# Kernel optimization log

Measured on AMD Instinct MI355X. Metric: run time of the kernel, lower is better.

Reference implementation:

```python
import jax, jax.numpy as jnp
import numpy as np

N = 100000   # nodes
E = 1600000  # edges
G = 512      # graphs
IN_F = 128
HID = 64
EPS = 1e-5


def setup_inputs() -> dict:
    key = jax.random.key(0)
    ks = jax.random.split(key, 16)
    x = jax.random.normal(ks[0], (N, IN_F), dtype=jnp.float32)
    edge_index = jax.random.randint(ks[1], (2, E), 0, N, dtype=jnp.int64)
    batch = jnp.sort(jax.random.randint(ks[2], (N,), 0, G, dtype=jnp.int64))
    s = 0.05
    return {
        'x': x, 'edge_index': edge_index, 'batch': batch,
        'W1': jax.random.normal(ks[3], (IN_F, HID), jnp.float32) * s,
        'b1': jax.random.normal(ks[4], (HID,), jnp.float32) * s,
        'g1': jax.random.uniform(ks[5], (HID,), jnp.float32),
        'be1': jax.random.normal(ks[6], (HID,), jnp.float32) * s,
        'rm1': jnp.zeros((HID,), jnp.float32),
        'rv1': jnp.ones((HID,), jnp.float32),
        'W2': jax.random.normal(ks[7], (HID, HID), jnp.float32) * s,
        'b2': jax.random.normal(ks[8], (HID,), jnp.float32) * s,
        'g2': jax.random.uniform(ks[9], (HID,), jnp.float32),
        'be2': jax.random.normal(ks[10], (HID,), jnp.float32) * s,
        'rm2': jnp.zeros((HID,), jnp.float32),
        'rv2': jnp.ones((HID,), jnp.float32),
        'Wh1': jax.random.normal(ks[11], (2 * HID, HID), jnp.float32) * s,
        'bh1': jax.random.normal(ks[12], (HID,), jnp.float32) * s,
        'Wh2': jax.random.normal(ks[13], (HID, HID // 2), jnp.float32) * s,
        'bh2': jnp.zeros((HID // 2,), jnp.float32),
        'Wh3': jax.random.normal(ks[14], (HID // 2, 1), jnp.float32) * s,
        'bh3': jnp.zeros((1,), jnp.float32),
    }


def _gcn(h, W, b, src, dst):
    # GCNConv with added self-loops and symmetric D^{-1/2} A D^{-1/2} normalization
    hw = h @ W                                   # [N, HID]
    deg = jnp.ones((N,), hw.dtype).at[dst].add(1.0)  # in-degree + self-loop
    dinv = jax.lax.rsqrt(deg)
    norm = dinv[src] * dinv[dst]                 # [E]
    agg = jax.ops.segment_sum(hw[src] * norm[:, None], dst, num_segments=N)
    return agg + hw * (dinv * dinv)[:, None] + b  # self-loop term + bias


def _bn(x, g, b, rm, rv):
    return (x - rm) * jax.lax.rsqrt(rv + EPS) * g + b


def reference(x, edge_index, batch, W1, b1, g1, be1, rm1, rv1,
              W2, b2, g2, be2, rm2, rv2, Wh1, bh1, Wh2, bh2, Wh3, bh3):
    src, dst = edge_index[0], edge_index[1]
    # layer 0 (no residual: dim change 128 -> 64)
    h = jax.nn.relu(_bn(_gcn(x, W1, b1, src, dst), g1, be1, rm1, rv1))
    # layer 1 with residual
    h = h + jax.nn.relu(_bn(_gcn(h, W2, b2, src, dst), g2, be2, rm2, rv2))
    # global mean + max pooling per graph
    ones = jnp.ones((N,), h.dtype)
    cnt = jnp.maximum(jax.ops.segment_sum(ones, batch, num_segments=G), 1.0)
    h_mean = jax.ops.segment_sum(h, batch, num_segments=G) / cnt[:, None]
    h_max = jax.ops.segment_max(h, batch, num_segments=G)
    hg = jnp.concatenate([h_mean, h_max], axis=-1)   # [G, 2*HID]
    # MLP head (dropout disabled in eval)
    z = jax.nn.relu(hg @ Wh1 + bh1)
    z = jax.nn.relu(z @ Wh2 + bh2)
    out = z @ Wh3 + bh3
    return jax.nn.sigmoid(out).squeeze(-1)           # [G]
```

## Files before the change

kernel.cpp:

```cpp
#include <hip/hip_runtime.h>
#include <math.h>

#define NN 100000
#define EE 1600000
#define GG 512
#define INF_ 128
#define HID 64
#define EPS 1e-5f

#define NBUK 391
#define P1_TILES 98

typedef unsigned int uint32;
typedef __attribute__((ext_vector_type(8))) short bf16x8;
typedef __attribute__((ext_vector_type(4))) float f32x4;

static __device__ inline uint32 f2bf(float f) {
    uint32 u = __float_as_uint(f);
    return (u + 0x7FFFu + ((u >> 16) & 1u)) >> 16;
}
static __device__ inline float bf_lo(uint32 u) { return __uint_as_float(u << 16); }
static __device__ inline float bf_hi(uint32 u) { return __uint_as_float(u & 0xFFFF0000u); }


__global__ __launch_bounds__(256) void k_bhist(const int* __restrict__ ei,
                                               int* __restrict__ bcnt) {
    __shared__ int h[NBUK];
    int t = threadIdx.x;
    for (int i = t; i < NBUK; i += 256) h[i] = 0;
    __syncthreads();
    const int4* dst4 = (const int4*)(ei + EE);
    int base4 = blockIdx.x * 4096;
    for (int j = 0; j < 16; ++j) {
        int i4 = base4 + j * 256 + t;
        if (i4 < EE / 4) {
            int4 d = dst4[i4];
            atomicAdd(&h[d.x >> 8], 1);
            atomicAdd(&h[d.y >> 8], 1);
            atomicAdd(&h[d.z >> 8], 1);
            atomicAdd(&h[d.w >> 8], 1);
        }
    }
    __syncthreads();
    for (int i = t; i < NBUK; i += 256)
        if (h[i]) atomicAdd(&bcnt[i], h[i]);
}

__global__ void k_bscan(const int* __restrict__ bcnt, int* __restrict__ bbase,
                        int* __restrict__ gcur, int* __restrict__ offs) {
    __shared__ int wsum[8];
    int t = threadIdx.x;
    int lane = t & 63, w = t >> 6;
    int c = (t < NBUK) ? bcnt[t] : 0;
    int v = c;
    for (int d = 1; d < 64; d <<= 1) { int n = __shfl_up(v, d); if (lane >= d) v += n; }
    if (lane == 63) wsum[w] = v;
    __syncthreads();
    int pre = 0;
    for (int q = 0; q < w; ++q) pre += wsum[q];
    int excl = pre + v - c;
    if (t <= NBUK) {
        bbase[t] = excl;
        if (t < NBUK) gcur[t] = excl;
    }
    if (t == 0) offs[NN] = EE;
}

__global__ __launch_bounds__(256) void k_p1(const int* __restrict__ ei,
                                            int* __restrict__ gcur,
                                            uint32* __restrict__ pairs) {
    __shared__ int h[NBUK];
    int t = threadIdx.x;
    for (int i = t; i < NBUK; i += 256) h[i] = 0;
    __syncthreads();
    const int4* src4 = (const int4*)ei;
    const int4* dst4 = (const int4*)(ei + EE);
    int base4 = blockIdx.x * 4096;
    for (int j = 0; j < 16; ++j) {
        int i4 = base4 + j * 256 + t;
        if (i4 < EE / 4) {
            int4 d = dst4[i4];
            atomicAdd(&h[d.x >> 8], 1);
            atomicAdd(&h[d.y >> 8], 1);
            atomicAdd(&h[d.z >> 8], 1);
            atomicAdd(&h[d.w >> 8], 1);
        }
    }
    __syncthreads();
    for (int i = t; i < NBUK; i += 256) {
        int c = h[i];
        h[i] = c ? atomicAdd(&gcur[i], c) : 0;
    }
    __syncthreads();
    for (int j = 0; j < 16; ++j) {
        int i4 = base4 + j * 256 + t;
        if (i4 < EE / 4) {
            int4 d = dst4[i4];
            int4 s = src4[i4];
            int p0 = atomicAdd(&h[d.x >> 8], 1);
            pairs[p0] = ((uint32)s.x << 8) | (uint32)(d.x & 255);
            int p1 = atomicAdd(&h[d.y >> 8], 1);
            pairs[p1] = ((uint32)s.y << 8) | (uint32)(d.y & 255);
            int p2 = atomicAdd(&h[d.z >> 8], 1);
            pairs[p2] = ((uint32)s.z << 8) | (uint32)(d.z & 255);
            int p3 = atomicAdd(&h[d.w >> 8], 1);
            pairs[p3] = ((uint32)s.w << 8) | (uint32)(d.w & 255);
        }
    }
}

__global__ __launch_bounds__(256) void k_p2(const uint32* __restrict__ pairs,
                                            const int* __restrict__ bbase,
                                            int* __restrict__ offs, float* __restrict__ dinv,
                                            int* __restrict__ col) {
    int b = blockIdx.x, t = threadIdx.x;
    int nbase = b << 8;
    int ebase = bbase[b], eend = bbase[b + 1];
    int m = eend - ebase;
    __shared__ int cnt[256];
    __shared__ int wsum[4];
    cnt[t] = 0;
    __syncthreads();
    for (int i = t; i < m; i += 256)
        atomicAdd(&cnt[pairs[ebase + i] & 255u], 1);
    __syncthreads();
    int c = cnt[t];
    int lane = t & 63, w = t >> 6;
    int v = c;
    for (int d = 1; d < 64; d <<= 1) { int n = __shfl_up(v, d); if (lane >= d) v += n; }
    if (lane == 63) wsum[w] = v;
    __syncthreads();
    int pre = 0;
    for (int q = 0; q < w; ++q) pre += wsum[q];
    int excl = pre + v - c;
    int node = nbase + t;
    if (node < NN) {
        offs[node] = ebase + excl;
        dinv[node] = rsqrtf(1.f + (float)c);
    }
    __syncthreads();
    cnt[t] = excl;
    __syncthreads();
    for (int i = t; i < m; i += 256) {
        uint32 u = pairs[ebase + i];
        int loc = atomicAdd(&cnt[u & 255u], 1);
        col[ebase + loc] = (int)(u >> 8);
    }
}

__global__ void k_setup(const float* b1, const float* g1, const float* be1,
                        const float* rm1, const float* rv1,
                        const float* b2, const float* g2, const float* be2,
                        const float* rm2, const float* rv2, float* sc,
                        const float* W1, uint32* Wt1b,
                        const float* W2, uint32* Wt2b, int* bcnt) {
    int i = blockIdx.x * 256 + threadIdx.x;
    if (i < 4096) {
        int n = i >> 6, kp = (i & 63) * 2;
        Wt1b[i] = f2bf(W1[(size_t)kp * 64 + n]) | (f2bf(W1[(size_t)(kp + 1) * 64 + n]) << 16);
    } else if (i < 6144) {
        int j = i - 4096;
        int n = j >> 5, kp = (j & 31) * 2;
        Wt2b[j] = f2bf(W2[(size_t)kp * 64 + n]) | (f2bf(W2[(size_t)(kp + 1) * 64 + n]) << 16);
    } else if (i < 6208) {
        int l = i - 6144;
        float s1 = g1[l] * rsqrtf(rv1[l] + EPS);
        sc[l]       = s1;
        sc[64 + l]  = (b1[l] - rm1[l]) * s1 + be1[l];
        float s2 = g2[l] * rsqrtf(rv2[l] + EPS);
        sc[128 + l] = s2;
        sc[192 + l] = (b2[l] - rm2[l]) * s2 + be2[l];
    } else if (i < 6208 + NBUK) {
        bcnt[i - 6208] = 0;
    }
}

template <int K>
__global__ __launch_bounds__(256) void k_gemm_mfma(const float* __restrict__ X,
                                                   const uint32* __restrict__ Wtb,
                                                   uint32* __restrict__ outb, int nrows) {
    constexpr int KP = K + 8;
    __shared__ alignas(16) unsigned short Al[64 * KP];
    __shared__ alignas(16) unsigned short Bl[64 * KP];
    int tid = threadIdx.x;
    for (int i = tid; i < 64 * (K / 2); i += 256) {
        int n = i / (K / 2), kp = i % (K / 2);
        *(uint32*)&Bl[n * KP + kp * 2] = Wtb[i];
    }
    int r0 = blockIdx.x * 64;
    const float* Xb = X + (size_t)r0 * K;
    int limit = (nrows - r0) * K;
    for (int f = tid * 4; f < 64 * K; f += 1024) {
        float4 v = {0.f, 0.f, 0.f, 0.f};
        if (f + 3 < limit) v = *(const float4*)&Xb[f];
        int row = f / K, kpos = f % K;
        ushort4 pk;
        pk.x = (unsigned short)f2bf(v.x);
        pk.y = (unsigned short)f2bf(v.y);
        pk.z = (unsigned short)f2bf(v.z);
        pk.w = (unsigned short)f2bf(v.w);
        *(ushort4*)&Al[row * KP + kpos] = pk;
    }
    __syncthreads();
    int lane = tid & 63, wv = tid >> 6;
    int m = lane & 15, quad = lane >> 4;
    f32x4 acc0 = {0.f, 0.f, 0.f, 0.f}, acc1 = acc0, acc2 = acc0, acc3 = acc0;
    int arow = wv * 16 + m;
#pragma unroll
    for (int k0 = 0; k0 < K; k0 += 32) {
        int koff = k0 + quad * 8;
        bf16x8 a = *(const bf16x8*)&Al[arow * KP + koff];
        bf16x8 b0 = *(const bf16x8*)&Bl[(0 * 16 + m) * KP + koff];
        bf16x8 b1 = *(const bf16x8*)&Bl[(1 * 16 + m) * KP + koff];
        bf16x8 b2 = *(const bf16x8*)&Bl[(2 * 16 + m) * KP + koff];
        bf16x8 b3 = *(const bf16x8*)&Bl[(3 * 16 + m) * KP + koff];
        acc0 = __builtin_amdgcn_mfma_f32_16x16x32_bf16(a, b0, acc0, 0, 0, 0);
        acc1 = __builtin_amdgcn_mfma_f32_16x16x32_bf16(a, b1, acc1, 0, 0, 0);
        acc2 = __builtin_amdgcn_mfma_f32_16x16x32_bf16(a, b2, acc2, 0, 0, 0);
        acc3 = __builtin_amdgcn_mfma_f32_16x16x32_bf16(a, b3, acc3, 0, 0, 0);
    }
    const float* accs[4] = {(const float*)&acc0, (const float*)&acc1,
                            (const float*)&acc2, (const float*)&acc3};
#pragma unroll
    for (int nt = 0; nt < 4; ++nt) {
#pragma unroll
        for (int reg = 0; reg < 4; ++reg) {
            float val = accs[nt][reg];
            float nxt = __shfl_down(val, 1);
            int row = r0 + wv * 16 + quad * 4 + reg;
            if (((m & 1) == 0) && row < nrows)
                outb[(size_t)row * 32 + nt * 8 + (m >> 1)] =
                    f2bf(val) | (f2bf(nxt) << 16);
        }
    }
}

__global__ void k_gcn_gather(const uint32* __restrict__ hwb, const int* __restrict__ col,
                             const int* __restrict__ offs,
                             const float* __restrict__ dinv, const float* __restrict__ scale,
                             const float* __restrict__ shift, const float* __restrict__ resid,
                             float* __restrict__ out) {
    int node = blockIdx.x * 4 + (threadIdx.x >> 6);
    if (node >= NN) return;
    int lane = threadIdx.x & 63;
    int half = lane >> 5;
    int fl = lane & 31;
    int e0 = offs[node], e1 = offs[node + 1];
    float di = dinv[node];
    float ax0 = 0.f, ay0 = 0.f, ax1 = 0.f, ay1 = 0.f;
    for (int base = e0; base < e1; base += 64) {
        int m = e1 - base; if (m > 64) m = 64;
        int srcv = 0; float wv = 0.f;
        if (lane < m) { srcv = col[base + lane]; wv = dinv[srcv]; }
        for (int j = 0; j < m; j += 8) {
            int   s0 = __shfl(srcv, j + half);
            int   s1 = __shfl(srcv, j + 2 + half);
            int   s2 = __shfl(srcv, j + 4 + half);
            int   s3 = __shfl(srcv, j + 6 + half);
            float w0 = __shfl(wv, j + half);
            float w1 = __shfl(wv, j + 2 + half);
            float w2 = __shfl(wv, j + 4 + half);
            float w3 = __shfl(wv, j + 6 + half);
            uint32 u0 = hwb[(size_t)s0 * 32 + fl];
            uint32 u1 = hwb[(size_t)s1 * 32 + fl];
            uint32 u2 = hwb[(size_t)s2 * 32 + fl];
            uint32 u3 = hwb[(size_t)s3 * 32 + fl];
            ax0 = fmaf(bf_lo(u0), w0, ax0); ay0 = fmaf(bf_hi(u0), w0, ay0);
            ax1 = fmaf(bf_lo(u1), w1, ax1); ay1 = fmaf(bf_hi(u1), w1, ay1);
            ax0 = fmaf(bf_lo(u2), w2, ax0); ay0 = fmaf(bf_hi(u2), w2, ay0);
            ax1 = fmaf(bf_lo(u3), w3, ax1); ay1 = fmaf(bf_hi(u3), w3, ay1);
        }
    }
    float ax = ax0 + ax1, ay = ay0 + ay1;
    ax += __shfl(ax, fl + 32);
    ay += __shfl(ay, fl + 32);
    if (half == 0) {
        uint32 uself = hwb[(size_t)node * 32 + fl];
        float dii = di * di;
        float vx = fmaf(ax * di + bf_lo(uself) * dii, scale[2 * fl],     shift[2 * fl]);
        float vy = fmaf(ay * di + bf_hi(uself) * dii, scale[2 * fl + 1], shift[2 * fl + 1]);
        vx = fmaxf(vx, 0.f);
        vy = fmaxf(vy, 0.f);
        if (resid) {
            float2 rv = *(const float2*)&resid[(size_t)node * 64 + 2 * fl];
            vx += rv.x; vy += rv.y;
        }
        float2 o; o.x = vx; o.y = vy;
        *(float2*)&out[(size_t)node * 64 + 2 * fl] = o;
    }
}

__global__ void k_pool(const float* __restrict__ h, const int* __restrict__ batch,
                       float* __restrict__ msum, float* __restrict__ mmax,
                       float* __restrict__ gcnt) {
    int lane = threadIdx.x;
    int i0 = blockIdx.x * 128;
    int i1 = i0 + 128; if (i1 > NN) i1 = NN;
    int cur = batch[i0];
    float sum = 0.f, mx = 0.f; int c = 0;
    for (int i = i0; i < i1; ++i) {
        int g = batch[i];
        if (g != cur) {
            atomicAdd(&msum[cur * 64 + lane], sum);
            atomicMax((unsigned int*)&mmax[cur * 64 + lane], __float_as_uint(mx));
            if (lane == 0) atomicAdd(&gcnt[cur], (float)c);
            sum = 0.f; mx = 0.f; c = 0; cur = g;
        }
        float v = h[(long)i * 64 + lane];
        sum += v; mx = fmaxf(mx, v); ++c;
    }
    atomicAdd(&msum[cur * 64 + lane], sum);
    atomicMax((unsigned int*)&mmax[cur * 64 + lane], __float_as_uint(mx));
    if (lane == 0) atomicAdd(&gcnt[cur], (float)c);
}

__global__ void k_head(const float* __restrict__ msum, const float* __restrict__ mmax,
                       const float* __restrict__ gcnt,
                       const float* __restrict__ Wh1, const float* __restrict__ bh1,
                       const float* __restrict__ Wh2, const float* __restrict__ bh2,
                       const float* __restrict__ Wh3, const float* __restrict__ bh3,
                       float* __restrict__ out) {
    int g = blockIdx.x, t = threadIdx.x;
    __shared__ float hg[128];
    __shared__ float z1[64];
    __shared__ float z2[32];
    float c = fmaxf(gcnt[g], 1.f);
    hg[t]      = msum[g * 64 + t] / c;
    hg[64 + t] = mmax[g * 64 + t];
    __syncthreads();
    float acc = bh1[t];
#pragma unroll 8
    for (int k = 0; k < 128; ++k) acc = fmaf(hg[k], Wh1[k * 64 + t], acc);
    z1[t] = fmaxf(acc, 0.f);
    __syncthreads();
    if (t < 32) {
        float a2 = bh2[t];
#pragma unroll 8
        for (int k = 0; k < 64; ++k) a2 = fmaf(z1[k], Wh2[k * 32 + t], a2);
        z2[t] = fmaxf(a2, 0.f);
    }
    __syncthreads();
    if (t == 0) {
        float a3 = bh3[0];
        for (int k = 0; k < 32; ++k) a3 = fmaf(z2[k], Wh3[k], a3);
        out[g] = 1.f / (1.f + expf(-a3));
    }
}


static inline size_t alignup(size_t x) { return (x + 255) & ~(size_t)255; }

extern "C" void kernel_launch(void* const* d_in, const int* in_sizes, int n_in,
                              void* d_out, int out_size, void* d_ws, size_t ws_size,
                              hipStream_t stream) {
    const float* x   = (const float*)d_in[0];
    const int*   ei  = (const int*)d_in[1];
    const int*   bat = (const int*)d_in[2];
    const float* W1  = (const float*)d_in[3];
    const float* b1  = (const float*)d_in[4];
    const float* g1  = (const float*)d_in[5];
    const float* be1 = (const float*)d_in[6];
    const float* rm1 = (const float*)d_in[7];
    const float* rv1 = (const float*)d_in[8];
    const float* W2  = (const float*)d_in[9];
    const float* b2  = (const float*)d_in[10];
    const float* g2  = (const float*)d_in[11];
    const float* be2 = (const float*)d_in[12];
    const float* rm2 = (const float*)d_in[13];
    const float* rv2 = (const float*)d_in[14];
    const float* Wh1 = (const float*)d_in[15];
    const float* bh1 = (const float*)d_in[16];
    const float* Wh2 = (const float*)d_in[17];
    const float* bh2 = (const float*)d_in[18];
    const float* Wh3 = (const float*)d_in[19];
    const float* bh3 = (const float*)d_in[20];
    float* out = (float*)d_out;

    char* ws = (char*)d_ws;
    size_t o = 0;
    int*   bcnt   = (int*)(ws + o);  o = alignup(o + NBUK * 4);
    int*   bbase  = (int*)(ws + o);  o = alignup(o + (NBUK + 1) * 4);
    int*   gcur   = (int*)(ws + o);  o = alignup(o + NBUK * 4);
    int*   offs   = (int*)(ws + o);  o = alignup(o + (NN + 1) * 4);
    uint32* pairs = (uint32*)(ws + o); o = alignup(o + (size_t)EE * 4);
    int*   col    = (int*)(ws + o);  o = alignup(o + (size_t)EE * 4);
    float* dinv   = (float*)(ws + o); o = alignup(o + (size_t)NN * 4);
    float* scb    = (float*)(ws + o); o = alignup(o + 4 * 64 * 4);
    uint32* Wt1b  = (uint32*)(ws + o); o = alignup(o + 64 * (INF_ / 2) * 4);
    uint32* Wt2b  = (uint32*)(ws + o); o = alignup(o + 64 * (HID / 2) * 4);
    float* msum   = (float*)(ws + o);
    size_t pool_off = o;              o += (size_t)GG * 64 * 4;
    float* mmax   = (float*)(ws + o); o += (size_t)GG * 64 * 4;
    float* gcnt   = (float*)(ws + o); o += (size_t)GG * 4;
    size_t pool_bytes = o - pool_off; o = alignup(o);
    uint32* hwb   = (uint32*)(ws + o); o = alignup(o + (size_t)NN * 32 * 4);
    float* h      = (float*)(ws + o); o = alignup(o + (size_t)NN * 64 * 4);
    (void)ws_size; (void)n_in; (void)in_sizes; (void)out_size;

    hipMemsetAsync(ws + pool_off, 0, pool_bytes, stream);

    k_setup<<<26, 256, 0, stream>>>(b1, g1, be1, rm1, rv1, b2, g2, be2, rm2, rv2,
                                    scb, W1, Wt1b, W2, Wt2b, bcnt);
    k_bhist<<<P1_TILES, 256, 0, stream>>>(ei, bcnt);
    k_bscan<<<1, 512, 0, stream>>>(bcnt, bbase, gcur, offs);
    k_p1<<<P1_TILES, 256, 0, stream>>>(ei, gcur, pairs);
    k_p2<<<NBUK, 256, 0, stream>>>(pairs, bbase, offs, dinv, col);

    k_gemm_mfma<INF_><<<(NN + 63) / 64, 256, 0, stream>>>(x, Wt1b, hwb, NN);
    k_gcn_gather<<<(NN + 3) / 4, 256, 0, stream>>>(hwb, col, offs, dinv,
                                                   scb, scb + 64, nullptr, h);
    k_gemm_mfma<HID><<<(NN + 63) / 64, 256, 0, stream>>>(h, Wt2b, hwb, NN);
    k_gcn_gather<<<(NN + 3) / 4, 256, 0, stream>>>(hwb, col, offs, dinv,
                                                   scb + 128, scb + 192, h, h);
    k_pool<<<(NN + 127) / 128, 64, 0, stream>>>(h, bat, msum, mmax, gcnt);
    k_head<<<GG, 64, 0, stream>>>(msum, mmax, gcnt, Wh1, bh1, Wh2, bh2, Wh3, bh3, out);
}
```

Baseline: 335.0 us.

## Fuse CSR histogram, setup, and pool zeroing; precompute per-block offsets; widen gather unroll

Merges the setup kernel, the bucket histogram and the pool-buffer memset into one launch that writes per-block histograms. A single scan kernel then computes exclusive per-block, per-bucket base offsets, so the scatter pass no longer recomputes its histogram or uses global atomics. The gather inner loop is unrolled to 16 edges per step for more loads in flight, and pooling uses 4 waves per block over 32-node chunks. Trade-offs: the scan runs serially over 98 blocks per bucket, the pool now does more atomic flushes, and the wider unroll raises register use.

```diff
diff --git a/kernel.cpp b/kernel.cpp
--- a/kernel.cpp
+++ b/kernel.cpp
@@ -10,6 +10,9 @@
 
 #define NBUK 391
 #define P1_TILES 98
+#define SETUP_B 25
+#define POOL_WORDS (GG * 64 * 2 + GG)
+#define ZERO_B ((POOL_WORDS + 255) / 256)
 
 typedef unsigned int uint32;
 typedef __attribute__((ext_vector_type(8))) short bf16x8;
@@ -23,35 +26,67 @@
 static __device__ inline float bf_hi(uint32 u) { return __uint_as_float(u & 0xFFFF0000u); }
 
 
-__global__ __launch_bounds__(256) void k_bhist(const int* __restrict__ ei,
-                                               int* __restrict__ bcnt) {
-    __shared__ int h[NBUK];
-    int t = threadIdx.x;
-    for (int i = t; i < NBUK; i += 256) h[i] = 0;
-    __syncthreads();
-    const int4* dst4 = (const int4*)(ei + EE);
-    int base4 = blockIdx.x * 4096;
-    for (int j = 0; j < 16; ++j) {
-        int i4 = base4 + j * 256 + t;
-        if (i4 < EE / 4) {
-            int4 d = dst4[i4];
-            atomicAdd(&h[d.x >> 8], 1);
-            atomicAdd(&h[d.y >> 8], 1);
-            atomicAdd(&h[d.z >> 8], 1);
-            atomicAdd(&h[d.w >> 8], 1);
-        }
-    }
-    __syncthreads();
-    for (int i = t; i < NBUK; i += 256)
-        if (h[i]) atomicAdd(&bcnt[i], h[i]);
-}
-
-__global__ void k_bscan(const int* __restrict__ bcnt, int* __restrict__ bbase,
-                        int* __restrict__ gcur, int* __restrict__ offs) {
+__global__ __launch_bounds__(256) void k_hist1(const int* __restrict__ ei,
+        int* __restrict__ hblk,
+        const float* b1, const float* g1, const float* be1,
+        const float* rm1, const float* rv1,
+        const float* b2, const float* g2, const float* be2,
+        const float* rm2, const float* rv2, float* sc,
+        const float* W1, uint32* Wt1b, const float* W2, uint32* Wt2b,
+        float* poolz) {
+    int b = blockIdx.x, t = threadIdx.x;
+    if (b < P1_TILES) {
+        __shared__ int h[NBUK];
+        for (int i = t; i < NBUK; i += 256) h[i] = 0;
+        __syncthreads();
+        const int4* dst4 = (const int4*)(ei + EE);
+        int base4 = b * 4096;
+        for (int j = 0; j < 16; ++j) {
+            int i4 = base4 + j * 256 + t;
+            if (i4 < EE / 4) {
+                int4 d = dst4[i4];
+                atomicAdd(&h[d.x >> 8], 1);
+                atomicAdd(&h[d.y >> 8], 1);
+                atomicAdd(&h[d.z >> 8], 1);
+                atomicAdd(&h[d.w >> 8], 1);
+            }
+        }
+        __syncthreads();
+        for (int i = t; i < NBUK; i += 256) hblk[b * NBUK + i] = h[i];
+    } else if (b < P1_TILES + SETUP_B) {
+        int i = (b - P1_TILES) * 256 + t;
+        if (i < 4096) {
+            int n = i >> 6, kp = (i & 63) * 2;
+            Wt1b[i] = f2bf(W1[(size_t)kp * 64 + n]) |
+                      (f2bf(W1[(size_t)(kp + 1) * 64 + n]) << 16);
+        } else if (i < 6144) {
+            int j = i - 4096;
+            int n = j >> 5, kp = (j & 31) * 2;
+            Wt2b[j] = f2bf(W2[(size_t)kp * 64 + n]) |
+                      (f2bf(W2[(size_t)(kp + 1) * 64 + n]) << 16);
+        } else if (i < 6208) {
+            int l = i - 6144;
+            float s1 = g1[l] * rsqrtf(rv1[l] + EPS);
+            sc[l]       = s1;
+            sc[64 + l]  = (b1[l] - rm1[l]) * s1 + be1[l];
+            float s2 = g2[l] * rsqrtf(rv2[l] + EPS);
+            sc[128 + l] = s2;
+            sc[192 + l] = (b2[l] - rm2[l]) * s2 + be2[l];
+        }
+    } else {
+        int i = (b - P1_TILES - SETUP_B) * 256 + t;
+        if (i < POOL_WORDS) poolz[i] = 0.f;
+    }
+}
+
+__global__ void k_scan2(const int* __restrict__ hblk, int* __restrict__ bbase,
+                        int* __restrict__ rbase, int* __restrict__ offs) {
     __shared__ int wsum[8];
     int t = threadIdx.x;
     int lane = t & 63, w = t >> 6;
-    int c = (t < NBUK) ? bcnt[t] : 0;
+    int c = 0;
+    if (t < NBUK)
+        for (int b = 0; b < P1_TILES; ++b) c += hblk[b * NBUK + t];
     int v = c;
     for (int d = 1; d < 64; d <<= 1) { int n = __shfl_up(v, d); if (lane >= d) v += n; }
     if (lane == 63) wsum[w] = v;
@@ -59,39 +94,27 @@
     int pre = 0;
     for (int q = 0; q < w; ++q) pre += wsum[q];
     int excl = pre + v - c;
-    if (t <= NBUK) {
-        bbase[t] = excl;
-        if (t < NBUK) gcur[t] = excl;
-    }
+    if (t <= NBUK) bbase[t] = excl;
     if (t == 0) offs[NN] = EE;
-}
-
-__global__ __launch_bounds__(256) void k_p1(const int* __restrict__ ei,
-                                            int* __restrict__ gcur,
-                                            uint32* __restrict__ pairs) {
+    if (t < NBUK) {
+        int run = excl;
+        for (int b = 0; b < P1_TILES; ++b) {
+            rbase[b * NBUK + t] = run;
+            run += hblk[b * NBUK + t];
+        }
+    }
+}
+
+__global__ __launch_bounds__(256) void k_p1b(const int* __restrict__ ei,
+                                             const int* __restrict__ rbase,
+                                             uint32* __restrict__ pairs) {
     __shared__ int h[NBUK];
-    int t = threadIdx.x;
-    for (int i = t; i < NBUK; i += 256) h[i] = 0;
+    int b = blockIdx.x, t = threadIdx.x;
+    for (int i = t; i < NBUK; i += 256) h[i] = rbase[b * NBUK + i];
     __syncthreads();
     const int4* src4 = (const int4*)ei;
     const int4* dst4 = (const int4*)(ei + EE);
-    int base4 = blockIdx.x * 4096;
-    for (int j = 0; j < 16; ++j) {
-        int i4 = base4 + j * 256 + t;
-        if (i4 < EE / 4) {
-            int4 d = dst4[i4];
-            atomicAdd(&h[d.x >> 8], 1);
-            atomicAdd(&h[d.y >> 8], 1);
-            atomicAdd(&h[d.z >> 8], 1);
-            atomicAdd(&h[d.w >> 8], 1);
-        }
-    }
-    __syncthreads();
-    for (int i = t; i < NBUK; i += 256) {
-        int c = h[i];
-        h[i] = c ? atomicAdd(&gcur[i], c) : 0;
-    }
-    __syncthreads();
+    int base4 = b * 4096;
     for (int j = 0; j < 16; ++j) {
         int i4 = base4 + j * 256 + t;
         if (i4 < EE / 4) {
@@ -145,33 +168,6 @@
         uint32 u = pairs[ebase + i];
         int loc = atomicAdd(&cnt[u & 255u], 1);
         col[ebase + loc] = (int)(u >> 8);
-    }
-}
-
-__global__ void k_setup(const float* b1, const float* g1, const float* be1,
-                        const float* rm1, const float* rv1,
-                        const float* b2, const float* g2, const float* be2,
-                        const float* rm2, const float* rv2, float* sc,
-                        const float* W1, uint32* Wt1b,
-                        const float* W2, uint32* Wt2b, int* bcnt) {
-    int i = blockIdx.x * 256 + threadIdx.x;
-    if (i < 4096) {
-        int n = i >> 6, kp = (i & 63) * 2;
-        Wt1b[i] = f2bf(W1[(size_t)kp * 64 + n]) | (f2bf(W1[(size_t)(kp + 1) * 64 + n]) << 16);
-    } else if (i < 6144) {
-        int j = i - 4096;
-        int n = j >> 5, kp = (j & 31) * 2;
-        Wt2b[j] = f2bf(W2[(size_t)kp * 64 + n]) | (f2bf(W2[(size_t)(kp + 1) * 64 + n]) << 16);
-    } else if (i < 6208) {
-        int l = i - 6144;
-        float s1 = g1[l] * rsqrtf(rv1[l] + EPS);
-        sc[l]       = s1;
-        sc[64 + l]  = (b1[l] - rm1[l]) * s1 + be1[l];
-        float s2 = g2[l] * rsqrtf(rv2[l] + EPS);
-        sc[128 + l] = s2;
-        sc[192 + l] = (b2[l] - rm2[l]) * s2 + be2[l];
-    } else if (i < 6208 + NBUK) {
-        bcnt[i - 6208] = 0;
     }
 }
 
@@ -252,23 +248,39 @@
         int m = e1 - base; if (m > 64) m = 64;
         int srcv = 0; float wv = 0.f;
         if (lane < m) { srcv = col[base + lane]; wv = dinv[srcv]; }
-        for (int j = 0; j < m; j += 8) {
+        for (int j = 0; j < m; j += 16) {
             int   s0 = __shfl(srcv, j + half);
             int   s1 = __shfl(srcv, j + 2 + half);
             int   s2 = __shfl(srcv, j + 4 + half);
             int   s3 = __shfl(srcv, j + 6 + half);
+            int   s4 = __shfl(srcv, j + 8 + half);
+            int   s5 = __shfl(srcv, j + 10 + half);
+            int   s6 = __shfl(srcv, j + 12 + half);
+            int   s7 = __shfl(srcv, j + 14 + half);
             float w0 = __shfl(wv, j + half);
             float w1 = __shfl(wv, j + 2 + half);
             float w2 = __shfl(wv, j + 4 + half);
             float w3 = __shfl(wv, j + 6 + half);
+            float w4 = __shfl(wv, j + 8 + half);
+            float w5 = __shfl(wv, j + 10 + half);
+            float w6 = __shfl(wv, j + 12 + half);
+            float w7 = __shfl(wv, j + 14 + half);
             uint32 u0 = hwb[(size_t)s0 * 32 + fl];
             uint32 u1 = hwb[(size_t)s1 * 32 + fl];
             uint32 u2 = hwb[(size_t)s2 * 32 + fl];
             uint32 u3 = hwb[(size_t)s3 * 32 + fl];
+            uint32 u4 = hwb[(size_t)s4 * 32 + fl];
+            uint32 u5 = hwb[(size_t)s5 * 32 + fl];
+            uint32 u6 = hwb[(size_t)s6 * 32 + fl];
+            uint32 u7 = hwb[(size_t)s7 * 32 + fl];
             ax0 = fmaf(bf_lo(u0), w0, ax0); ay0 = fmaf(bf_hi(u0), w0, ay0);
             ax1 = fmaf(bf_lo(u1), w1, ax1); ay1 = fmaf(bf_hi(u1), w1, ay1);
             ax0 = fmaf(bf_lo(u2), w2, ax0); ay0 = fmaf(bf_hi(u2), w2, ay0);
             ax1 = fmaf(bf_lo(u3), w3, ax1); ay1 = fmaf(bf_hi(u3), w3, ay1);
+            ax0 = fmaf(bf_lo(u4), w4, ax0); ay0 = fmaf(bf_hi(u4), w4, ay0);
+            ax1 = fmaf(bf_lo(u5), w5, ax1); ay1 = fmaf(bf_hi(u5), w5, ay1);
+            ax0 = fmaf(bf_lo(u6), w6, ax0); ay0 = fmaf(bf_hi(u6), w6, ay0);
+            ax1 = fmaf(bf_lo(u7), w7, ax1); ay1 = fmaf(bf_hi(u7), w7, ay1);
         }
     }
     float ax = ax0 + ax1, ay = ay0 + ay1;
@@ -290,12 +302,15 @@
     }
 }
 
-__global__ void k_pool(const float* __restrict__ h, const int* __restrict__ batch,
+__global__ __launch_bounds__(256) void k_pool(const float* __restrict__ h,
+                       const int* __restrict__ batch,
                        float* __restrict__ msum, float* __restrict__ mmax,
                        float* __restrict__ gcnt) {
-    int lane = threadIdx.x;
-    int i0 = blockIdx.x * 128;
-    int i1 = i0 + 128; if (i1 > NN) i1 = NN;
+    int lane = threadIdx.x & 63;
+    int wv = threadIdx.x >> 6;
+    int i0 = blockIdx.x * 128 + wv * 32;
+    if (i0 >= NN) return;
+    int i1 = i0 + 32; if (i1 > NN) i1 = NN;
     int cur = batch[i0];
     float sum = 0.f, mx = 0.f; int c = 0;
     for (int i = i0; i < i1; ++i) {
@@ -378,9 +393,9 @@
 
     char* ws = (char*)d_ws;
     size_t o = 0;
-    int*   bcnt   = (int*)(ws + o);  o = alignup(o + NBUK * 4);
+    int*   hblk   = (int*)(ws + o);  o = alignup(o + (size_t)P1_TILES * NBUK * 4);
+    int*   rbase  = (int*)(ws + o);  o = alignup(o + (size_t)P1_TILES * NBUK * 4);
     int*   bbase  = (int*)(ws + o);  o = alignup(o + (NBUK + 1) * 4);
-    int*   gcur   = (int*)(ws + o);  o = alignup(o + NBUK * 4);
     int*   offs   = (int*)(ws + o);  o = alignup(o + (NN + 1) * 4);
     uint32* pairs = (uint32*)(ws + o); o = alignup(o + (size_t)EE * 4);
     int*   col    = (int*)(ws + o);  o = alignup(o + (size_t)EE * 4);
@@ -388,22 +403,19 @@
     float* scb    = (float*)(ws + o); o = alignup(o + 4 * 64 * 4);
     uint32* Wt1b  = (uint32*)(ws + o); o = alignup(o + 64 * (INF_ / 2) * 4);
     uint32* Wt2b  = (uint32*)(ws + o); o = alignup(o + 64 * (HID / 2) * 4);
-    float* msum   = (float*)(ws + o);
-    size_t pool_off = o;              o += (size_t)GG * 64 * 4;
+    float* msum   = (float*)(ws + o); o += (size_t)GG * 64 * 4;
     float* mmax   = (float*)(ws + o); o += (size_t)GG * 64 * 4;
     float* gcnt   = (float*)(ws + o); o += (size_t)GG * 4;
-    size_t pool_bytes = o - pool_off; o = alignup(o);
+    o = alignup(o);
     uint32* hwb   = (uint32*)(ws + o); o = alignup(o + (size_t)NN * 32 * 4);
     float* h      = (float*)(ws + o); o = alignup(o + (size_t)NN * 64 * 4);
     (void)ws_size; (void)n_in; (void)in_sizes; (void)out_size;
 
-    hipMemsetAsync(ws + pool_off, 0, pool_bytes, stream);
-
-    k_setup<<<26, 256, 0, stream>>>(b1, g1, be1, rm1, rv1, b2, g2, be2, rm2, rv2,
-                                    scb, W1, Wt1b, W2, Wt2b, bcnt);
-    k_bhist<<<P1_TILES, 256, 0, stream>>>(ei, bcnt);
-    k_bscan<<<1, 512, 0, stream>>>(bcnt, bbase, gcur, offs);
-    k_p1<<<P1_TILES, 256, 0, stream>>>(ei, gcur, pairs);
+    k_hist1<<<P1_TILES + SETUP_B + ZERO_B, 256, 0, stream>>>(
+        ei, hblk, b1, g1, be1, rm1, rv1, b2, g2, be2, rm2, rv2, scb,
+        W1, Wt1b, W2, Wt2b, msum);
+    k_scan2<<<1, 512, 0, stream>>>(hblk, bbase, rbase, offs);
+    k_p1b<<<P1_TILES, 256, 0, stream>>>(ei, rbase, pairs);
     k_p2<<<NBUK, 256, 0, stream>>>(pairs, bbase, offs, dinv, col);
 
     k_gemm_mfma<INF_><<<(NN + 63) / 64, 256, 0, stream>>>(x, Wt1b, hwb, NN);
@@ -412,6 +424,6 @@
     k_gemm_mfma<HID><<<(NN + 63) / 64, 256, 0, stream>>>(h, Wt2b, hwb, NN);
     k_gcn_gather<<<(NN + 3) / 4, 256, 0, stream>>>(hwb, col, offs, dinv,
                                                    scb + 128, scb + 192, h, h);
-    k_pool<<<(NN + 127) / 128, 64, 0, stream>>>(h, bat, msum, mmax, gcnt);
+    k_pool<<<(NN + 127) / 128, 256, 0, stream>>>(h, bat, msum, mmax, gcnt);
     k_head<<<GG, 64, 0, stream>>>(msum, mmax, gcnt, Wh1, bh1, Wh2, bh2, Wh3, bh3, out);
 }
```

Result: faster. 303.3 us (-9.5%).
